# Performance work log

Hardware: AMD Instinct MI355X
Metric: run time of the kernel (lower is better)

## Reference

```python
import jax, jax.numpy as jnp
import numpy as np

L = 16                      # number of hash-grid levels
T = 2 ** 14                 # max entries per level
F = 2                       # features per level
B_GROWTH = np.exp((np.log(512.0) - np.log(16.0)) / (L - 1))
NS = [int(16 * B_GROWTH ** i) for i in range(L)]  # 16,20,25,...,512
PRIMES = np.array([1, 2654435761, 805459861], dtype=np.uint32)
# vertex_offsets[i] = [i>>2 & 1, i>>1 & 1, i & 1]
OFF = np.array([[(i >> (2 - j)) & 1 for j in range(3)] for i in range(8)], dtype=np.int32)
OFF_F = OFF.astype(np.float32)
BB_MIN, BB_SIZE = -5.0, 10.0


def hash_encode(x3, embed):
    """x3: [B,3] float32, embed: [L,T,F]. Returns [B, L*F]."""
    scaled = (x3 - BB_MIN) / BB_SIZE
    clamped = jnp.clip(scaled, 0.0, 1.0 - 1e-6)
    off = jnp.asarray(OFF)            # [8,3] int32
    off_f = jnp.asarray(OFF_F)        # [8,3] float32
    primes = jnp.asarray(PRIMES)      # [3] uint32
    outs = []
    for l in range(L):
        n_l = NS[l]
        x_l = clamped * n_l                       # [B,3]
        fl = jnp.floor(x_l)
        verts = fl.astype(jnp.int32)[:, None, :] + off[None]  # [B,8,3]
        if (n_l + 1) ** 3 <= T:
            idx = (verts[:, :, 0] * (n_l + 1) ** 2
                   + verts[:, :, 1] * (n_l + 1)
                   + verts[:, :, 2])              # [B,8] dense index
        else:
            v = verts.astype(jnp.uint32)
            h = (v[:, :, 0] * primes[0]) ^ (v[:, :, 1] * primes[1]) ^ (v[:, :, 2] * primes[2])
            idx = (h & (T - 1)).astype(jnp.int32)  # mod 2^14 (power of two)
        w = x_l - fl                               # [B,3] fractional part
        # trilinear weights: prod over 3 dims of (off*w + (1-off)*(1-w))
        w8 = jnp.prod(off_f[None] * w[:, None, :] + (1.0 - off_f[None]) * (1.0 - w[:, None, :]), axis=2)  # [B,8]
        feats = embed[l][idx]                      # [B,8,F] gather
        outs.append(jnp.sum(feats * w8[:, :, None], axis=1))  # [B,F]
    return jnp.concatenate(outs, axis=1)           # [B, L*F]


def setup_inputs() -> dict:
    key = jax.random.key(0)
    ks = jax.random.split(key, 16)
    B = 2097152
    hidden = 64
    x3 = jax.random.uniform(ks[0], (B, 3), jnp.float32) * 10.0 - 5.0   # points in bb
    vd = jax.random.normal(ks[1], (B, 3), jnp.float32)                 # view directions
    x = jnp.concatenate([x3, vd], axis=1)
    embed = jax.random.uniform(ks[2], (L, T, F), jnp.float32, -1e-4, 1e-4)
    def lin(k, fan_in, fan_out):
        k1, k2 = jax.random.split(k)
        bound = 1.0 / np.sqrt(fan_in)
        W = jax.random.uniform(k1, (fan_in, fan_out), jnp.float32, -bound, bound)
        b = jax.random.uniform(k2, (fan_out,), jnp.float32, -bound, bound)
        return W, b
    dW0, db0 = lin(ks[3], L * F, hidden)
    dW1, db1 = lin(ks[4], hidden, hidden // 4)
    cW0, cb0 = lin(ks[5], 3 + hidden // 4, hidden)
    cW1, cb1 = lin(ks[6], hidden, hidden)
    cW2, cb2 = lin(ks[7], hidden, 3)
    return {"x": x, "embed": embed,
            "dW0": dW0, "db0": db0, "dW1": dW1, "db1": db1,
            "cW0": cW0, "cb0": cb0, "cW1": cW1, "cb1": cb1, "cW2": cW2, "cb2": cb2}


def reference(x, embed, dW0, db0, dW1, db1, cW0, cb0, cW1, cb1, cW2, cb2):
    pts = hash_encode(x[:, :3], embed)                       # [B,32]
    view = x[:, 3:]                                          # [B,3]
    h = jax.nn.relu(pts @ dW0 + db0) @ dW1 + db1             # [B,16]
    density = jax.nn.sigmoid(h[:, :1])                       # [B,1]
    h_rest = jax.nn.relu(h[:, 1:])                           # [B,15]
    c = jnp.concatenate([density, h_rest, view], axis=-1)    # [B,19]
    c = jax.nn.relu(c @ cW0 + cb0)
    c = jax.nn.relu(c @ cW1 + cb1)
    color = jax.nn.sigmoid(c @ cW2 + cb2)                    # [B,3]
    return jnp.concatenate([density, color], axis=-1)        # [B,4]
```

## Files before the change

kernel.cpp:

```cpp
#include <hip/hip_runtime.h>
#include <math.h>

#define NLEVEL 16
#define TSIZE 16384
#define ESTRIDE 32768

using half4 = __attribute__((ext_vector_type(4))) _Float16;
using f32x4 = __attribute__((ext_vector_type(4))) float;
using f32x2 = __attribute__((ext_vector_type(2))) float;
using u32x2 = __attribute__((ext_vector_type(2))) unsigned;
typedef __fp16 hv2 __attribute__((ext_vector_type(2)));

struct NsParam { int n[NLEVEL]; unsigned densemask; };

union Frag { half4 v; int i[2]; };
union Hu { unsigned u; hv2 h; };

__device__ __forceinline__ Frag load_wfrag(const float* __restrict__ W, int ldn,
                                           int k0, int q, int out,
                                           int kmax, int omax) {
    Frag f;
    #pragma unroll
    for (int j = 0; j < 4; ++j) {
        int k = k0 + 4 * q + j;
        float v = (k < kmax && out < omax) ? W[k * ldn + out] : 0.0f;
        f.v[j] = (_Float16)v;
    }
    return f;
}

__device__ __forceinline__ f32x4 mfma16(const Frag& a, const Frag& b, f32x4 c) {
    return __builtin_amdgcn_mfma_f32_16x16x16f16(a.v, b.v, c, 0, 0, 0);
}

__device__ __forceinline__ Frag actpack(f32x4 a) {
    Frag f;
    #pragma unroll
    for (int j = 0; j < 4; ++j) f.v[j] = (_Float16)fmaxf(a[j], 0.0f);
    return f;
}

__device__ __forceinline__ float sigmoidf(float x) {
    return 1.0f / (1.0f + expf(-x));
}

__device__ __forceinline__ int qsel(int q, int a, int b, int c, int d) {
    return (q & 2) ? ((q & 1) ? d : c) : ((q & 1) ? b : a);
}

__device__ __forceinline__ unsigned pkrtz(float a, float b) {
    union { hv2 h; unsigned u; } r;
    r.h = __builtin_amdgcn_cvt_pkrtz(a, b);
    return r.u;
}

__device__ __forceinline__ hv2 splath(float w) {
    Hu r; r.u = pkrtz(w, w); return r.h;
}

__device__ __forceinline__ hv2 hlerp(hv2 a, hv2 b, hv2 w) {
    return (hv2)((b - a) * w + a);
}


__device__ __forceinline__ void gather_issue(
    const unsigned* __restrict__ tab,
    float cxp, float cyp, float czp,
    float fn, int np1, int np1sq, int dense,
    unsigned fe[8], float& w0, float& w1, float& w2)
{
    float xl0 = cxp * fn, xl1 = cyp * fn, xl2 = czp * fn;
    float f0 = floorf(xl0), f1 = floorf(xl1), f2 = floorf(xl2);
    int i0 = (int)f0, i1 = (int)f1, i2 = (int)f2;
    w0 = xl0 - f0; w1 = xl1 - f1; w2 = xl2 - f2;
    if (dense) {
        int d000 = i0 * np1sq + i1 * np1 + i2;
        #pragma unroll
        for (int c = 0; c < 8; ++c) {
            int o0 = (c >> 2) & 1, o1 = (c >> 1) & 1, o2 = c & 1;
            fe[c] = tab[d000 + (o0 ? np1sq : 0) + (o1 ? np1 : 0) + o2];
        }
    } else {
        unsigned hx0 = (unsigned)i0, hx1 = hx0 + 1u;
        unsigned hy0 = (unsigned)i1 * 2654435761u, hy1 = hy0 + 2654435761u;
        unsigned hz0 = (unsigned)i2 * 805459861u,  hz1 = hz0 + 805459861u;
        #pragma unroll
        for (int c = 0; c < 8; ++c) {
            int o0 = (c >> 2) & 1, o1 = (c >> 1) & 1, o2 = c & 1;
            unsigned h = (o0 ? hx1 : hx0) ^ (o1 ? hy1 : hy0) ^ (o2 ? hz1 : hz0);
            fe[c] = tab[h & (TSIZE - 1)];
        }
    }
}

__device__ __forceinline__ unsigned interp_tree(
    const unsigned fe[8], float w0, float w1, float w2)
{
    hv2 W0 = splath(w0), W1 = splath(w1), W2 = splath(w2);
    Hu a, b;
    a.u = fe[0]; b.u = fe[1]; hv2 g00 = hlerp(a.h, b.h, W2);
    a.u = fe[2]; b.u = fe[3]; hv2 g01 = hlerp(a.h, b.h, W2);
    a.u = fe[4]; b.u = fe[5]; hv2 g10 = hlerp(a.h, b.h, W2);
    a.u = fe[6]; b.u = fe[7]; hv2 g11 = hlerp(a.h, b.h, W2);
    hv2 gy0 = hlerp(g00, g01, W1);
    hv2 gy1 = hlerp(g10, g11, W1);
    Hu r; r.h = hlerp(gy0, gy1, W0);
    return r.u;
}

__device__ __forceinline__ void loadc4(
    const float* __restrict__ x, int g0, int chunk, int B,
    float cx[4], float cy[4], float cz[4])
{
    #pragma unroll
    for (int p = 0; p < 4; ++p) {
        int idx = g0 + (chunk * 4 + p) * ESTRIDE;
        idx = (idx < B) ? idx : (B - 1);
        const float* xp = x + (size_t)idx * 6;
        f32x2 a = *(const f32x2*)xp;
        float pz = xp[2];
        cx[p] = fminf(fmaxf((a.x + 5.0f) / 10.0f, 0.0f), 0.999999f);
        cy[p] = fminf(fmaxf((a.y + 5.0f) / 10.0f, 0.0f), 0.999999f);
        cz[p] = fminf(fmaxf((pz  + 5.0f) / 10.0f, 0.0f), 0.999999f);
    }
}

__device__ __forceinline__ void enc_chunk(
    const unsigned* __restrict__ tab, unsigned* __restrict__ wplane,
    int g0, int chunk, int B,
    const float cx[4], const float cy[4], const float cz[4],
    float fn, int np1, int np1sq, int dense)
{
    unsigned fe[2][8];
    float w0s[2], w1s[2], w2s[2];
    gather_issue(tab, cx[0], cy[0], cz[0], fn, np1, np1sq, dense,
                 fe[0], w0s[0], w1s[0], w2s[0]);
    #pragma unroll
    for (int p = 0; p < 4; ++p) {
        if (p + 1 < 4)
            gather_issue(tab, cx[p + 1], cy[p + 1], cz[p + 1],
                         fn, np1, np1sq, dense,
                         fe[(p + 1) & 1], w0s[(p + 1) & 1],
                         w1s[(p + 1) & 1], w2s[(p + 1) & 1]);
        unsigned pk = interp_tree(fe[p & 1], w0s[p & 1], w1s[p & 1], w2s[p & 1]);
        int idx = g0 + (chunk * 4 + p) * ESTRIDE;
        if (idx < B) wplane[idx] = pk;
    }
}

__global__ __launch_bounds__(1024, 8) void nerf_encode(
    const float* __restrict__ x,
    const float* __restrict__ embed,
    unsigned* __restrict__ ws, int B, NsParam ns)
{
    __shared__ unsigned tab[TSIZE];
    const int tid = threadIdx.x;
    const int l = blockIdx.x & 15;
    const int slice = blockIdx.x >> 4;

    {
        const f32x4* src = (const f32x4*)(embed + (size_t)l * (TSIZE * 2));
        #pragma unroll
        for (int j = 0; j < 8; ++j) {
            f32x4 v = src[tid + 1024 * j];
            u32x2 pk;
            pk.x = pkrtz(v.x, v.y);
            pk.y = pkrtz(v.z, v.w);
            *(u32x2*)(tab + 2 * (tid + 1024 * j)) = pk;
        }
    }
    __syncthreads();

    const int n = ns.n[l];
    const float fn = (float)n;
    const int np1 = n + 1, np1sq = np1 * np1;
    const int dense = (ns.densemask >> l) & 1;
    unsigned* __restrict__ wplane = ws + (size_t)l * B;

    const int g0 = slice * 1024 + tid;
    const int nIter = (B + ESTRIDE - 1) / ESTRIDE;
    const int NC = (nIter + 3) >> 2;

    float cxA[4], cyA[4], czA[4], cxB[4], cyB[4], czB[4];
    loadc4(x, g0, 0, B, cxA, cyA, czA);
    for (int c = 0; c < NC; c += 2) {
        loadc4(x, g0, c + 1, B, cxB, cyB, czB);
        enc_chunk(tab, wplane, g0, c, B, cxA, cyA, czA, fn, np1, np1sq, dense);
        loadc4(x, g0, c + 2, B, cxA, cyA, czA);
        if (c + 1 < NC)
            enc_chunk(tab, wplane, g0, c + 1, B, cxB, cyB, czB,
                      fn, np1, np1sq, dense);
    }
}

struct Pre { Frag f0[2], f1[2]; float vx[2], vy[2], vz[2]; };

__device__ __forceinline__ void prefetch_tile(
    const unsigned* __restrict__ ws, int B, int q,
    const float* __restrict__ x, int tile32, int pt, Pre& P)
{
    const unsigned* pl0 = ws + (size_t)(2 * q) * B;
    const unsigned* pl1 = ws + (size_t)(2 * q + 1) * B;
    const unsigned* pl2 = ws + (size_t)(8 + 2 * q) * B;
    const unsigned* pl3 = ws + (size_t)(9 + 2 * q) * B;
    #pragma unroll
    for (int g = 0; g < 2; ++g) {
        int ptg = tile32 * 32 + g * 16 + pt;
        P.f0[g].i[0] = (int)__builtin_nontemporal_load(pl0 + ptg);
        P.f0[g].i[1] = (int)__builtin_nontemporal_load(pl1 + ptg);
        P.f1[g].i[0] = (int)__builtin_nontemporal_load(pl2 + ptg);
        P.f1[g].i[1] = (int)__builtin_nontemporal_load(pl3 + ptg);
        const float* xp = x + (size_t)ptg * 6;
        P.vx[g] = xp[3];
        f32x2 v45 = *(const f32x2*)(xp + 4);
        P.vy[g] = v45.x; P.vz[g] = v45.y;
    }
}

__global__ __launch_bounds__(256, 4) void nerf_mlp(
    const float* __restrict__ x,
    const unsigned* __restrict__ ws,
    const float* __restrict__ dW0, const float* __restrict__ db0,
    const float* __restrict__ dW1, const float* __restrict__ db1,
    const float* __restrict__ cW0, const float* __restrict__ cb0,
    const float* __restrict__ cW1, const float* __restrict__ cb1,
    const float* __restrict__ cW2, const float* __restrict__ cb2,
    float* __restrict__ out, int B)
{
    const int lane = threadIdx.x & 63;
    const int pt = lane & 15;
    const int q  = lane >> 4;
    const int tid = threadIdx.x;
    const int wavesPerBlock = blockDim.x >> 6;
    const int waveId = blockIdx.x * wavesPerBlock + (threadIdx.x >> 6);
    const int waveStride = gridDim.x * wavesPerBlock;
    const int numT = B >> 5;

    __shared__ Frag wldsC0[8][64];
    __shared__ Frag wldsC1[16][64];
    __shared__ f32x4 blds[14][4];
    for (int e = tid; e < 8 * 64; e += 256) {
        int f = e >> 6, ln = e & 63;
        wldsC0[f][ln] = load_wfrag(cW0, 64, 16 * (f & 1), ln >> 4,
                                   16 * (f >> 1) + (ln & 15), 19, 64);
    }
    for (int e = tid; e < 16 * 64; e += 256) {
        int f = e >> 6, ln = e & 63;
        wldsC1[f][ln] = load_wfrag(cW1, 64, 16 * (f & 3), ln >> 4,
                                   16 * (f >> 2) + (ln & 15), 64, 64);
    }
    if (tid < 56) {
        int f = tid >> 2, qq = tid & 3;
        f32x4 v;
        if (f < 4)       v = *(const f32x4*)(db0 + 16 * f + 4 * qq);
        else if (f == 4) v = *(const f32x4*)(db1 + 4 * qq);
        else if (f < 9)  v = *(const f32x4*)(cb0 + 16 * (f - 5) + 4 * qq);
        else if (f < 13) v = *(const f32x4*)(cb1 + 16 * (f - 9) + 4 * qq);
        else {
            v[0] = (qq == 0) ? cb2[0] : 0.0f;
            v[1] = (qq == 0) ? cb2[1] : 0.0f;
            v[2] = (qq == 0) ? cb2[2] : 0.0f;
            v[3] = 0.0f;
        }
        blds[f][qq] = v;
    }

    Frag wdW0[4][2], wdW1[4], wcW2[4];
    #pragma unroll
    for (int t = 0; t < 4; ++t)
        #pragma unroll
        for (int c = 0; c < 2; ++c)
            wdW0[t][c] = load_wfrag(dW0, 64, 16 * c, q, 16 * t + pt, 32, 64);
    #pragma unroll
    for (int c = 0; c < 4; ++c)
        wdW1[c] = load_wfrag(dW1, 16, 16 * c, q, pt, 64, 16);
    #pragma unroll
    for (int c = 0; c < 4; ++c)
        wcW2[c] = load_wfrag(cW2, 3, 16 * c, q, pt, 64, 3);

    __syncthreads();

    int tile = waveId;
    if (tile >= numT) return;

    Pre P;
    prefetch_tile(ws, B, q, x, tile, pt, P);

    for (;;) {
        int next = tile + waveStride;
        bool hasNext = next < numT;

        Frag bf0[2] = { P.f0[0], P.f0[1] };
        Frag bf1[2] = { P.f1[0], P.f1[1] };
        float vx[2] = { P.vx[0], P.vx[1] };
        float vy[2] = { P.vy[0], P.vy[1] };
        float vz[2] = { P.vz[0], P.vz[1] };
        const int ptbase = tile * 32;

        if (hasNext) prefetch_tile(ws, B, q, x, next, pt, P);

        int wl = lane, wq = q;
        asm("" : "+v"(wl));
        asm("" : "+v"(wq));

        __builtin_amdgcn_s_setprio(1);

        f32x4 acc[2][4];
        #pragma unroll
        for (int t = 0; t < 4; ++t) {
            f32x4 b = blds[t][wq];
            #pragma unroll
            for (int g = 0; g < 2; ++g) {
                f32x4 a = b;
                a = mfma16(wdW0[t][0], bf0[g], a);
                a = mfma16(wdW0[t][1], bf1[g], a);
                acc[g][t] = a;
            }
        }
        Frag bh[2][4];
        #pragma unroll
        for (int c = 0; c < 4; ++c)
            #pragma unroll
            for (int g = 0; g < 2; ++g) bh[g][c] = actpack(acc[g][c]);

        f32x4 bl1 = blds[4][wq];
        f32x4 h[2] = { bl1, bl1 };
        #pragma unroll
        for (int c = 0; c < 4; ++c)
            #pragma unroll
            for (int g = 0; g < 2; ++g) h[g] = mfma16(wdW1[c], bh[g][c], h[g]);

        float dens[2];
        Frag bcin0[2], bcin1[2];
        #pragma unroll
        for (int g = 0; g < 2; ++g) {
            dens[g] = sigmoidf(h[g][0]);
            float a0v = (q == 0) ? dens[g] : fmaxf(h[g][0], 0.0f);
            bcin0[g].v[0] = (_Float16)a0v;
            bcin0[g].v[1] = (_Float16)fmaxf(h[g][1], 0.0f);
            bcin0[g].v[2] = (_Float16)fmaxf(h[g][2], 0.0f);
            bcin0[g].v[3] = (_Float16)fmaxf(h[g][3], 0.0f);
            bcin1[g].v[0] = (_Float16)((q == 0) ? vx[g] : 0.0f);
            bcin1[g].v[1] = (_Float16)((q == 0) ? vy[g] : 0.0f);
            bcin1[g].v[2] = (_Float16)((q == 0) ? vz[g] : 0.0f);
            bcin1[g].v[3] = (_Float16)0.0f;
        }

        #pragma unroll
        for (int t = 0; t < 4; ++t) {
            f32x4 b = blds[5 + t][wq];
            Frag w0f = wldsC0[2 * t + 0][wl];
            Frag w1f = wldsC0[2 * t + 1][wl];
            #pragma unroll
            for (int g = 0; g < 2; ++g) {
                f32x4 a = b;
                a = mfma16(w0f, bcin0[g], a);
                a = mfma16(w1f, bcin1[g], a);
                acc[g][t] = a;
            }
        }
        Frag bc[2][4];
        #pragma unroll
        for (int c = 0; c < 4; ++c)
            #pragma unroll
            for (int g = 0; g < 2; ++g) bc[g][c] = actpack(acc[g][c]);

        #pragma unroll
        for (int t = 0; t < 4; ++t) {
            f32x4 b = blds[9 + t][wq];
            #pragma unroll
            for (int g = 0; g < 2; ++g) acc[g][t] = b;
            #pragma unroll
            for (int c = 0; c < 4; ++c) {
                Frag wf = wldsC1[4 * t + c][wl];
                #pragma unroll
                for (int g = 0; g < 2; ++g)
                    acc[g][t] = mfma16(wf, bc[g][c], acc[g][t]);
            }
        }
        Frag bd[2][4];
        #pragma unroll
        for (int c = 0; c < 4; ++c)
            #pragma unroll
            for (int g = 0; g < 2; ++g) bd[g][c] = actpack(acc[g][c]);

        f32x4 bl4 = blds[13][wq];
        f32x4 fo[2] = { bl4, bl4 };
        #pragma unroll
        for (int c = 0; c < 4; ++c)
            #pragma unroll
            for (int g = 0; g < 2; ++g) fo[g] = mfma16(wcW2[c], bd[g][c], fo[g]);

        __builtin_amdgcn_s_setprio(0);

        if (q == 0) {
            #pragma unroll
            for (int g = 0; g < 2; ++g) {
                f32x4 o;
                o[0] = dens[g];
                o[1] = sigmoidf(fo[g][0]);
                o[2] = sigmoidf(fo[g][1]);
                o[3] = sigmoidf(fo[g][2]);
                __builtin_nontemporal_store(o,
                    (f32x4*)(out + (size_t)(ptbase + g * 16 + pt) * 4));
            }
        }

        if (!hasNext) break;
        tile = next;
    }
}

__device__ __forceinline__ void opaque(const float*& p) {
    asm("" : "+v"(p));
}

__device__ __forceinline__ void enc_issue(
    float px, float py, float pz,
    const float fn_[4], const float* const eb_[4],
    const int np1_[4], const int np1sq_[4], const bool dense_[4],
    f32x2 fe[4][8], float w_[4][3])
{
    float cx = fminf(fmaxf((px + 5.0f) / 10.0f, 0.0f), 0.999999f);
    float cy = fminf(fmaxf((py + 5.0f) / 10.0f, 0.0f), 0.999999f);
    float cz = fminf(fmaxf((pz + 5.0f) / 10.0f, 0.0f), 0.999999f);

    #pragma unroll
    for (int d = 0; d < 4; ++d) {
        float fn = fn_[d];
        float xl0 = cx * fn, xl1 = cy * fn, xl2 = cz * fn;
        float f0 = floorf(xl0), f1 = floorf(xl1), f2 = floorf(xl2);
        int i0 = (int)f0, i1 = (int)f1, i2 = (int)f2;
        w_[d][0] = xl0 - f0; w_[d][1] = xl1 - f1; w_[d][2] = xl2 - f2;

        unsigned hx0 = (unsigned)i0, hx1 = hx0 + 1u;
        unsigned hy0 = (unsigned)i1 * 2654435761u, hy1 = hy0 + 2654435761u;
        unsigned hz0 = (unsigned)i2 * 805459861u,  hz1 = hz0 + 805459861u;
        int dx0 = 0, dx1 = 0, dy0 = 0, dy1 = 0;
        if (d < 2) {
            dx0 = i0 * np1sq_[d]; dx1 = dx0 + np1sq_[d];
            dy0 = i1 * np1_[d];   dy1 = dy0 + np1_[d];
        }
        #pragma unroll
        for (int c = 0; c < 8; ++c) {
            int o0 = (c >> 2) & 1, o1 = (c >> 1) & 1, o2 = c & 1;
            unsigned h = (o0 ? hx1 : hx0) ^ (o1 ? hy1 : hy0) ^ (o2 ? hz1 : hz0);
            int ind = (int)(h & (TSIZE - 1));
            if (d < 2) {
                int di = (o0 ? dx1 : dx0) + (o1 ? dy1 : dy0) + i2 + o2;
                ind = dense_[d] ? di : ind;
            }
            fe[d][c] = *(const f32x2*)(eb_[d] + (size_t)ind * 2);
        }
    }
}

__global__ __launch_bounds__(256) void nerf_fused(
    const float* __restrict__ x,
    const float* __restrict__ embed,
    const float* __restrict__ dW0, const float* __restrict__ db0,
    const float* __restrict__ dW1, const float* __restrict__ db1,
    const float* __restrict__ cW0, const float* __restrict__ cb0,
    const float* __restrict__ cW1, const float* __restrict__ cb1,
    const float* __restrict__ cW2, const float* __restrict__ cb2,
    float* __restrict__ out, int B, NsParam ns)
{
    const int lane = threadIdx.x & 63;
    const int pt = lane & 15;
    const int q  = lane >> 4;
    const int wavesPerBlock = blockDim.x >> 6;
    const int waveId = blockIdx.x * wavesPerBlock + (threadIdx.x >> 6);
    const int waveStride = gridDim.x * wavesPerBlock;
    const int numTiles = B >> 4;

    Frag wdW0[4][2], wdW1[4], wcW0[4][2], wcW1[4][4], wcW2[4];
    #pragma unroll
    for (int t = 0; t < 4; ++t)
        #pragma unroll
        for (int c = 0; c < 2; ++c)
            wdW0[t][c] = load_wfrag(dW0, 64, 16 * c, q, 16 * t + pt, 32, 64);
    #pragma unroll
    for (int c = 0; c < 4; ++c)
        wdW1[c] = load_wfrag(dW1, 16, 16 * c, q, pt, 64, 16);
    #pragma unroll
    for (int t = 0; t < 4; ++t)
        #pragma unroll
        for (int c = 0; c < 2; ++c)
            wcW0[t][c] = load_wfrag(cW0, 64, 16 * c, q, 16 * t + pt, 19, 64);
    #pragma unroll
    for (int t = 0; t < 4; ++t)
        #pragma unroll
        for (int c = 0; c < 4; ++c)
            wcW1[t][c] = load_wfrag(cW1, 64, 16 * c, q, 16 * t + pt, 64, 64);
    #pragma unroll
    for (int c = 0; c < 4; ++c)
        wcW2[c] = load_wfrag(cW2, 3, 16 * c, q, pt, 64, 3);

    float fn_[4];
    const float* eb_[4];
    int np1_[4], np1sq_[4];
    bool dense_[4];
    #pragma unroll
    for (int d = 0; d < 4; ++d) {
        int base = (d < 2) ? (d) : (8 + (d - 2));
        int lvl = base + 2 * q;
        int n = qsel(q, ns.n[base], ns.n[base + 2], ns.n[base + 4], ns.n[base + 6]);
        fn_[d] = (float)n;
        np1_[d] = n + 1;
        np1sq_[d] = (n + 1) * (n + 1);
        dense_[d] = (ns.densemask >> lvl) & 1u;
        eb_[d] = embed + (size_t)lvl * (TSIZE * 2);
    }

    for (int tile = waveId; tile < numTiles; tile += waveStride) {
        const int ptg = tile * 16 + pt;
        const float* xp = x + (size_t)ptg * 6;
        f32x2 x01 = *(const f32x2*)(xp);
        f32x2 x23 = *(const f32x2*)(xp + 2);
        f32x2 x45 = *(const f32x2*)(xp + 4);
        float vx = x23.y, vy = x45.x, vz = x45.y;

        f32x2 fe[4][8];
        float w_[4][3];
        enc_issue(x01.x, x01.y, x23.x, fn_, eb_, np1_, np1sq_, dense_, fe, w_);

        Frag bf0, bf1;
        #pragma unroll
        for (int d = 0; d < 4; ++d) {
            float w0 = w_[d][0], w1 = w_[d][1], w2 = w_[d][2];
            float u0 = 1.0f - w0, u1 = 1.0f - w1, u2 = 1.0f - w2;
            float wxy[4] = { u0 * u1, u0 * w1, w0 * u1, w0 * w1 };
            float a0 = 0.0f, a1 = 0.0f;
            #pragma unroll
            for (int c = 0; c < 8; ++c) {
                float ww = wxy[c >> 1] * ((c & 1) ? w2 : u2);
                a0 = fmaf(fe[d][c].x, ww, a0);
                a1 = fmaf(fe[d][c].y, ww, a1);
            }
            if (d == 0)      { bf0.v[0] = (_Float16)a0; bf0.v[1] = (_Float16)a1; }
            else if (d == 1) { bf0.v[2] = (_Float16)a0; bf0.v[3] = (_Float16)a1; }
            else if (d == 2) { bf1.v[0] = (_Float16)a0; bf1.v[1] = (_Float16)a1; }
            else             { bf1.v[2] = (_Float16)a0; bf1.v[3] = (_Float16)a1; }
        }

        const float* db0o = db0; const float* db1o = db1;
        const float* cb0o = cb0; const float* cb1o = cb1;
        const float* cb2o = cb2;
        opaque(db0o); opaque(db1o); opaque(cb0o); opaque(cb1o); opaque(cb2o);

        f32x4 acc[4];
        #pragma unroll
        for (int t = 0; t < 4; ++t) {
            acc[t] = *(const f32x4*)(db0o + 16 * t + 4 * q);
            acc[t] = mfma16(wdW0[t][0], bf0, acc[t]);
            acc[t] = mfma16(wdW0[t][1], bf1, acc[t]);
        }
        Frag bh[4];
        #pragma unroll
        for (int c = 0; c < 4; ++c) bh[c] = actpack(acc[c]);

        f32x4 h = *(const f32x4*)(db1o + 4 * q);
        #pragma unroll
        for (int c = 0; c < 4; ++c) h = mfma16(wdW1[c], bh[c], h);

        float dens = sigmoidf(h[0]);
        Frag bcin0, bcin1;
        {
            float a0v = (q == 0) ? dens : fmaxf(h[0], 0.0f);
            bcin0.v[0] = (_Float16)a0v;
            bcin0.v[1] = (_Float16)fmaxf(h[1], 0.0f);
            bcin0.v[2] = (_Float16)fmaxf(h[2], 0.0f);
            bcin0.v[3] = (_Float16)fmaxf(h[3], 0.0f);
            bcin1.v[0] = (_Float16)((q == 0) ? vx : 0.0f);
            bcin1.v[1] = (_Float16)((q == 0) ? vy : 0.0f);
            bcin1.v[2] = (_Float16)((q == 0) ? vz : 0.0f);
            bcin1.v[3] = (_Float16)0.0f;
        }

        #pragma unroll
        for (int t = 0; t < 4; ++t) {
            acc[t] = *(const f32x4*)(cb0o + 16 * t + 4 * q);
            acc[t] = mfma16(wcW0[t][0], bcin0, acc[t]);
            acc[t] = mfma16(wcW0[t][1], bcin1, acc[t]);
        }
        Frag bc[4];
        #pragma unroll
        for (int c = 0; c < 4; ++c) bc[c] = actpack(acc[c]);

        #pragma unroll
        for (int t = 0; t < 4; ++t) {
            acc[t] = *(const f32x4*)(cb1o + 16 * t + 4 * q);
            #pragma unroll
            for (int c = 0; c < 4; ++c) acc[t] = mfma16(wcW1[t][c], bc[c], acc[t]);
        }
        Frag bd[4];
        #pragma unroll
        for (int c = 0; c < 4; ++c) bd[c] = actpack(acc[c]);

        float b0 = cb2o[0], b1 = cb2o[1], b2 = cb2o[2];
        f32x4 fo;
        fo[0] = (q == 0) ? b0 : 0.0f;
        fo[1] = (q == 0) ? b1 : 0.0f;
        fo[2] = (q == 0) ? b2 : 0.0f;
        fo[3] = 0.0f;
        #pragma unroll
        for (int c = 0; c < 4; ++c) fo = mfma16(wcW2[c], bd[c], fo);

        if (q == 0) {
            f32x4 o;
            o[0] = dens;
            o[1] = sigmoidf(fo[0]);
            o[2] = sigmoidf(fo[1]);
            o[3] = sigmoidf(fo[2]);
            *(f32x4*)(out + (size_t)ptg * 4) = o;
        }
    }
}

extern "C" void kernel_launch(void* const* d_in, const int* in_sizes, int n_in,
                              void* d_out, int out_size, void* d_ws, size_t ws_size,
                              hipStream_t stream) {
    const float* x    = (const float*)d_in[0];
    const float* embed= (const float*)d_in[1];
    const float* dW0  = (const float*)d_in[2];
    const float* db0  = (const float*)d_in[3];
    const float* dW1  = (const float*)d_in[4];
    const float* db1  = (const float*)d_in[5];
    const float* cW0  = (const float*)d_in[6];
    const float* cb0  = (const float*)d_in[7];
    const float* cW1  = (const float*)d_in[8];
    const float* cb1  = (const float*)d_in[9];
    const float* cW2  = (const float*)d_in[10];
    const float* cb2  = (const float*)d_in[11];
    float* out = (float*)d_out;

    int B = in_sizes[0] / 6;

    NsParam ns;
    double g = exp((log(512.0) - log(16.0)) / 15.0);
    ns.densemask = 0;
    for (int i = 0; i < NLEVEL; ++i) {
        ns.n[i] = (int)(16.0 * pow(g, (double)i));
        long long np1 = ns.n[i] + 1;
        if (np1 * np1 * np1 <= TSIZE) ns.densemask |= (1u << i);
    }

    size_t wsNeed = (size_t)NLEVEL * (size_t)B * 4;
    if (ws_size >= wsNeed && d_ws != nullptr && (B & 31) == 0 && B >= 32) {
        unsigned* ws = (unsigned*)d_ws;
        nerf_encode<<<512, 1024, 0, stream>>>(x, embed, ws, B, ns);
        nerf_mlp<<<2048, 256, 0, stream>>>(x, ws,
            dW0, db0, dW1, db1, cW0, cb0, cW1, cb1, cW2, cb2, out, B);
    } else {
        nerf_fused<<<2048, 256, 0, stream>>>(x, embed,
            dW0, db0, dW1, db1, cW0, cb0, cW1, cb1, cW2, cb2, out, B, ns);
    }
}
```

Baseline: 284.3 us.

## Double encode grid, precompute byte-offset hash addressing, nontemporal workspace stores

The encode kernel now launches 1024 blocks instead of 512, with the element stride doubled to match, so each block stages its level table and then processes half as many points. Hash and dense indices are computed directly as byte offsets, and the eight hashed corners are derived by XOR-ing per-axis deltas, which cuts per-corner integer ALU and shift work. Workspace writes become nontemporal stores to reduce cache pollution before the MLP pass reads them. The trade-off is that each level's 64KB table is loaded into LDS twice as often.

Result: no change. 288.4 us (+1.4%).

```diff
diff --git a/kernel.cpp b/kernel.cpp
--- a/kernel.cpp
+++ b/kernel.cpp
@@ -3,7 +3,7 @@
 
 #define NLEVEL 16
 #define TSIZE 16384
-#define ESTRIDE 32768
+#define ESTRIDE 65536
 
 using half4 = __attribute__((ext_vector_type(4))) _Float16;
 using f32x4 = __attribute__((ext_vector_type(4))) float;
@@ -66,30 +66,41 @@
 __device__ __forceinline__ void gather_issue(
     const unsigned* __restrict__ tab,
     float cxp, float cyp, float czp,
-    float fn, int np1, int np1sq, int dense,
+    float fn, int np1b, int np1sqb, int dense,
     unsigned fe[8], float& w0, float& w1, float& w2)
 {
     float xl0 = cxp * fn, xl1 = cyp * fn, xl2 = czp * fn;
     float f0 = floorf(xl0), f1 = floorf(xl1), f2 = floorf(xl2);
     int i0 = (int)f0, i1 = (int)f1, i2 = (int)f2;
     w0 = xl0 - f0; w1 = xl1 - f1; w2 = xl2 - f2;
+    const char* tb = (const char*)tab;
     if (dense) {
-        int d000 = i0 * np1sq + i1 * np1 + i2;
+        int b000 = i0 * np1sqb + i1 * np1b + (i2 << 2);
         #pragma unroll
         for (int c = 0; c < 8; ++c) {
             int o0 = (c >> 2) & 1, o1 = (c >> 1) & 1, o2 = c & 1;
-            fe[c] = tab[d000 + (o0 ? np1sq : 0) + (o1 ? np1 : 0) + o2];
+            int off = b000 + (o0 ? np1sqb : 0) + (o1 ? np1b : 0) + (o2 << 2);
+            fe[c] = *(const unsigned*)(tb + off);
         }
     } else {
-        unsigned hx0 = (unsigned)i0, hx1 = hx0 + 1u;
-        unsigned hy0 = (unsigned)i1 * 2654435761u, hy1 = hy0 + 2654435761u;
-        unsigned hz0 = (unsigned)i2 * 805459861u,  hz1 = hz0 + 805459861u;
-        #pragma unroll
-        for (int c = 0; c < 8; ++c) {
-            int o0 = (c >> 2) & 1, o1 = (c >> 1) & 1, o2 = c & 1;
-            unsigned h = (o0 ? hx1 : hx0) ^ (o1 ? hy1 : hy0) ^ (o2 ? hz1 : hz0);
-            fe[c] = tab[h & (TSIZE - 1)];
-        }
+        unsigned HX = (unsigned)i0 << 2;
+        unsigned HY = (unsigned)i1 * (2654435761u << 2);
+        unsigned HZ = (unsigned)i2 * (805459861u << 2);
+        unsigned A  = HX ^ HY ^ HZ;
+        unsigned DX = HX ^ (HX + 4u);
+        unsigned DY = HY ^ (HY + (2654435761u << 2));
+        unsigned DZ = HZ ^ (HZ + (805459861u << 2));
+        const unsigned mask = (TSIZE - 1) << 2;
+        unsigned b00 = A,        b10 = A ^ DX;
+        unsigned b01 = b00 ^ DY, b11 = b10 ^ DY;
+        fe[0] = *(const unsigned*)(tb + (b00 & mask));
+        fe[1] = *(const unsigned*)(tb + ((b00 ^ DZ) & mask));
+        fe[2] = *(const unsigned*)(tb + (b01 & mask));
+        fe[3] = *(const unsigned*)(tb + ((b01 ^ DZ) & mask));
+        fe[4] = *(const unsigned*)(tb + (b10 & mask));
+        fe[5] = *(const unsigned*)(tb + ((b10 ^ DZ) & mask));
+        fe[6] = *(const unsigned*)(tb + (b11 & mask));
+        fe[7] = *(const unsigned*)(tb + ((b11 ^ DZ) & mask));
     }
 }
 
@@ -129,22 +140,22 @@
     const unsigned* __restrict__ tab, unsigned* __restrict__ wplane,
     int g0, int chunk, int B,
     const float cx[4], const float cy[4], const float cz[4],
-    float fn, int np1, int np1sq, int dense)
+    float fn, int np1b, int np1sqb, int dense)
 {
     unsigned fe[2][8];
     float w0s[2], w1s[2], w2s[2];
-    gather_issue(tab, cx[0], cy[0], cz[0], fn, np1, np1sq, dense,
+    gather_issue(tab, cx[0], cy[0], cz[0], fn, np1b, np1sqb, dense,
                  fe[0], w0s[0], w1s[0], w2s[0]);
     #pragma unroll
     for (int p = 0; p < 4; ++p) {
         if (p + 1 < 4)
             gather_issue(tab, cx[p + 1], cy[p + 1], cz[p + 1],
-                         fn, np1, np1sq, dense,
+                         fn, np1b, np1sqb, dense,
                          fe[(p + 1) & 1], w0s[(p + 1) & 1],
                          w1s[(p + 1) & 1], w2s[(p + 1) & 1]);
         unsigned pk = interp_tree(fe[p & 1], w0s[p & 1], w1s[p & 1], w2s[p & 1]);
         int idx = g0 + (chunk * 4 + p) * ESTRIDE;
-        if (idx < B) wplane[idx] = pk;
+        if (idx < B) __builtin_nontemporal_store(pk, wplane + idx);
     }
 }
 
@@ -173,7 +184,7 @@
 
     const int n = ns.n[l];
     const float fn = (float)n;
-    const int np1 = n + 1, np1sq = np1 * np1;
+    const int np1b = (n + 1) << 2, np1sqb = (n + 1) * (n + 1) << 2;
     const int dense = (ns.densemask >> l) & 1;
     unsigned* __restrict__ wplane = ws + (size_t)l * B;
 
@@ -185,11 +196,11 @@
     loadc4(x, g0, 0, B, cxA, cyA, czA);
     for (int c = 0; c < NC; c += 2) {
         loadc4(x, g0, c + 1, B, cxB, cyB, czB);
-        enc_chunk(tab, wplane, g0, c, B, cxA, cyA, czA, fn, np1, np1sq, dense);
+        enc_chunk(tab, wplane, g0, c, B, cxA, cyA, czA, fn, np1b, np1sqb, dense);
         loadc4(x, g0, c + 2, B, cxA, cyA, czA);
         if (c + 1 < NC)
             enc_chunk(tab, wplane, g0, c + 1, B, cxB, cyB, czB,
-                      fn, np1, np1sq, dense);
+                      fn, np1b, np1sqb, dense);
     }
 }
 
@@ -648,7 +659,7 @@
     size_t wsNeed = (size_t)NLEVEL * (size_t)B * 4;
     if (ws_size >= wsNeed && d_ws != nullptr && (B & 31) == 0 && B >= 32) {
         unsigned* ws = (unsigned*)d_ws;
-        nerf_encode<<<512, 1024, 0, stream>>>(x, embed, ws, B, ns);
+        nerf_encode<<<1024, 1024, 0, stream>>>(x, embed, ws, B, ns);
         nerf_mlp<<<2048, 256, 0, stream>>>(x, ws,
             dW0, db0, dW1, db1, cW0, cb0, cW1, cb1, cW2, cb2, out, B);
     } else {
```
